# Optimization experiments

Hardware: AMD Instinct MI355X
Metric: run time of the kernel (lower is better)

## Reference

```python
import jax, jax.numpy as jnp
import numpy as np

N_NODES = 50000
N_EDGES = 800000
D_IN = 128
D_OUT = 128
BN_EPS = 1e-5


def setup_inputs() -> dict:
    key = jax.random.key(0)
    ks = jax.random.split(key, 8)
    node_feats = jax.random.normal(ks[0], (N_NODES, D_IN), dtype=jnp.float32)
    src = jax.random.randint(ks[1], (N_EDGES,), 0, N_NODES, dtype=jnp.int32)
    dst = jax.random.randint(ks[2], (N_EDGES,), 0, N_NODES, dtype=jnp.int32)
    # Glorot-ish init for weights
    scale = 1.0 / np.sqrt(D_IN)
    W = jax.random.normal(ks[3], (D_IN, D_OUT), dtype=jnp.float32) * scale
    b = jnp.zeros((D_OUT,), dtype=jnp.float32)
    Wr = jax.random.normal(ks[4], (D_IN, D_OUT), dtype=jnp.float32) * scale
    br = jnp.zeros((D_OUT,), dtype=jnp.float32)
    gamma = jnp.ones((D_OUT,), dtype=jnp.float32)
    beta = jnp.zeros((D_OUT,), dtype=jnp.float32)
    return {"node_feats": node_feats, "src": src, "dst": dst, "W": W, "b": b,
            "Wr": Wr, "br": br, "gamma": gamma, "beta": beta}


def reference(node_feats, src, dst, W, b, Wr, br, gamma, beta):
    N = node_feats.shape[0]
    ones_e = jnp.ones(src.shape[0], dtype=node_feats.dtype)
    # DGL GraphConv norm='both': D_out^{-1/2} on source side, D_in^{-1/2} on dest side
    deg_out = jnp.clip(jax.ops.segment_sum(ones_e, src, num_segments=N), 1.0)
    deg_in = jnp.clip(jax.ops.segment_sum(ones_e, dst, num_segments=N), 1.0)
    h = node_feats * jax.lax.rsqrt(deg_out)[:, None]        # [N, D_in]
    agg = jax.ops.segment_sum(h[src], dst, num_segments=N)  # gather + scatter-add, [N, D_in]
    agg = agg * jax.lax.rsqrt(deg_in)[:, None]
    gcn = jax.nn.relu(agg @ W + b)                           # GraphConv activation=relu
    res = jax.nn.relu(node_feats @ Wr + br)                  # residual branch
    y = gcn + res
    # BatchNorm1d (training mode: biased batch stats)
    mean = jnp.mean(y, axis=0)
    var = jnp.mean(jnp.square(y - mean), axis=0)
    out = (y - mean) * jax.lax.rsqrt(var + BN_EPS) * gamma + beta
    return out
```

## Files before the change

kernel.cpp:

```cpp
#include <hip/hip_runtime.h>

#define N_NODES 50000
#define N_EDGES 800000
#define D 128
#define BN_EPS 1e-5f
#define AGG_BLOCKS 2048
#define CHUNKS 64
#define EPC (N_EDGES / CHUNKS)
#define EPC4 (EPC / 4)
#define HALF_BINS 25600
#define HALF_U32 12800
#define QUART_BINS 12800
#define QUART_U32 6400
#define NB_MERGE 100

typedef short bf16x8 __attribute__((ext_vector_type(8)));
typedef float f32x4  __attribute__((ext_vector_type(4)));
typedef float f32x2  __attribute__((ext_vector_type(2)));
typedef unsigned int u32x4 __attribute__((ext_vector_type(4)));
typedef int i32x4 __attribute__((ext_vector_type(4)));


__device__ __forceinline__ unsigned int pack_rne(float a, float b) {
    unsigned int ua = __float_as_uint(a); ua += 0x7fffu + ((ua >> 16) & 1u);
    unsigned int ub = __float_as_uint(b); ub += 0x7fffu + ((ub >> 16) & 1u);
    return (ua >> 16) | (ub & 0xffff0000u);
}
__device__ __forceinline__ unsigned short pack1_rne(float a) {
    unsigned int ua = __float_as_uint(a); ua += 0x7fffu + ((ua >> 16) & 1u);
    return (unsigned short)(ua >> 16);
}
__device__ __forceinline__ unsigned char pack1_fp8(float a) {
    unsigned int u = __builtin_amdgcn_cvt_pk_fp8_f32(a, a, 0, false);
    return (unsigned char)(u & 0xffu);
}

__device__ __forceinline__ void scan_blksum(const int* __restrict__ blk_sum,
                                            int* sh, int t) {
    int v = (t < NB_MERGE) ? blk_sum[t] : 0;
    if (t < 256) sh[t] = v;
    __syncthreads();
    int inc = v;
    #pragma unroll
    for (int off = 1; off < 256; off <<= 1) {
        int u = (t >= off && t < 256) ? sh[t - off] : 0;
        __syncthreads();
        inc += u;
        if (t < 256) sh[t] = inc;
        __syncthreads();
    }
}
#define BLK_OFF(sh, mb) ((mb) ? (sh)[(mb) - 1] : 0)

__global__ __launch_bounds__(256) void hist_kernel(
        const int* __restrict__ dst, const int* __restrict__ src,
        unsigned int* __restrict__ histD, unsigned int* __restrict__ histS,
        const float* __restrict__ W, const float* __restrict__ Wr,
        uint4* __restrict__ pW, uint4* __restrict__ pWr) {
    __shared__ unsigned int h[HALF_U32];
    int tid = threadIdx.x;
    int c = blockIdx.x, r = blockIdx.y;
    if (c >= CHUNKS) {
        if (r != 0 || blockIdx.z != 0) return;
        int t = (c - CHUNKS) * 256 + tid;
        const float* S = (t & 2048) ? Wr : W;
        uint4* Dst     = (t & 2048) ? pWr : pW;
        int e = t & 2047;
        int lane = e & 63, ks = (e >> 6) & 3, ct = e >> 8;
        int n  = ct * 16 + (lane & 15);
        int k0 = ks * 32 + (lane >> 4) * 8;
        float v[8];
        #pragma unroll
        for (int j = 0; j < 8; j++) v[j] = S[(k0 + j) * D + n];
        uint4 rr;
        rr.x = pack_rne(v[0], v[1]); rr.y = pack_rne(v[2], v[3]);
        rr.z = pack_rne(v[4], v[5]); rr.w = pack_rne(v[6], v[7]);
        Dst[e] = rr;
        return;
    }
    const int* keys = blockIdx.z ? src : dst;
    unsigned int* hist = blockIdx.z ? histS : histD;
    for (int j = tid; j < HALF_U32; j += 256) h[j] = 0u;
    __syncthreads();
    int lo = r * HALF_BINS;
    const i32x4* keys4 = (const i32x4*)(keys + c * EPC);
    for (int i = tid; i < EPC4; i += 256) {
        i32x4 k = __builtin_nontemporal_load(keys4 + i);
        int b0 = k.x - lo, b1 = k.y - lo, b2 = k.z - lo, b3 = k.w - lo;
        if ((unsigned)b0 < (unsigned)HALF_BINS) atomicAdd(&h[b0 >> 1], 1u << ((b0 & 1) * 16));
        if ((unsigned)b1 < (unsigned)HALF_BINS) atomicAdd(&h[b1 >> 1], 1u << ((b1 & 1) * 16));
        if ((unsigned)b2 < (unsigned)HALF_BINS) atomicAdd(&h[b2 >> 1], 1u << ((b2 & 1) * 16));
        if ((unsigned)b3 < (unsigned)HALF_BINS) atomicAdd(&h[b3 >> 1], 1u << ((b3 & 1) * 16));
    }
    __syncthreads();
    unsigned int* out = hist + ((size_t)(r * CHUNKS + c)) * HALF_U32;
    for (int j = tid; j < HALF_U32; j += 256) out[j] = h[j];
}

__global__ __launch_bounds__(256) void merge_kernel(
        unsigned int* __restrict__ histD, unsigned int* __restrict__ histS,
        int* __restrict__ cnt_in, int* __restrict__ cnt_out,
        int* __restrict__ row_ptr, int* __restrict__ blk_sum) {
    __shared__ int sh[256];
    int t = threadIdx.x;
    int bx = blockIdx.x;
    int r = bx / 50;
    int q = (bx % 50) * 256 + t;
    int n0 = r * HALF_BINS + q * 2;
    if (blockIdx.y) {
        size_t base = (size_t)r * CHUNKS * HALF_U32 + q;
        unsigned int vals[CHUNKS];
        #pragma unroll
        for (int c = 0; c < CHUNKS; c++)
            vals[c] = histS[base + (size_t)c * HALF_U32];
        unsigned int lo = 0, hi = 0;
        #pragma unroll
        for (int c = 0; c < CHUNKS; c++) {
            lo += vals[c] & 0xffffu; hi += vals[c] >> 16;
        }
        cnt_out[n0]     = (int)lo;
        cnt_out[n0 + 1] = (int)hi;
        return;
    }
    size_t base = (size_t)r * CHUNKS * HALF_U32 + q;
    unsigned int vals[CHUNKS];
    #pragma unroll
    for (int c = 0; c < CHUNKS; c++)
        vals[c] = histD[base + (size_t)c * HALF_U32];
    unsigned int lo = 0, hi = 0;
    #pragma unroll
    for (int c = 0; c < CHUNKS; c++) {
        unsigned int v = vals[c];
        histD[base + (size_t)c * HALF_U32] = lo | (hi << 16);
        lo += v & 0xffffu; hi += v >> 16;
    }
    cnt_in[n0]     = (int)lo;
    cnt_in[n0 + 1] = (int)hi;
    int pair = (int)lo + (int)hi;
    sh[t] = pair;
    __syncthreads();
    int inc = pair;
    #pragma unroll
    for (int off = 1; off < 256; off <<= 1) {
        int u = (t >= off) ? sh[t - off] : 0;
        __syncthreads();
        inc += u; sh[t] = inc;
        __syncthreads();
    }
    int excl = inc - pair;
    row_ptr[n0]     = excl;
    row_ptr[n0 + 1] = excl + (int)lo;
    if (t == 255) blk_sum[bx] = inc;
}

__global__ __launch_bounds__(512) void fill2_kernel(
        const int* __restrict__ src, const int* __restrict__ dst,
        const int* __restrict__ row_ptr, const unsigned int* __restrict__ histP,
        const int* __restrict__ blk_sum, int* __restrict__ csr_src) {
    __shared__ unsigned int h[QUART_U32];
    __shared__ int sho[256];
    int tid = threadIdx.x;
    scan_blksum(blk_sum, sho, tid);
    int c = blockIdx.x, s = blockIdx.y;
    int base = c * EPC;
    for (int j = tid; j < QUART_U32; j += 512) h[j] = 0u;
    __syncthreads();
    int lo = s * QUART_BINS;
    int r = s >> 1;
    const unsigned int* pre_c = histP + ((size_t)(r * CHUNKS + c)) * HALF_U32
                                      + (s & 1) * QUART_U32;
    for (int i = tid; i < EPC; i += 512) {
        int d = __builtin_nontemporal_load(dst + base + i);
        int b = d - lo;
        if ((unsigned)b < (unsigned)QUART_BINS) {
            int shft = (b & 1) * 16;
            unsigned int old = atomicAdd(&h[b >> 1], 1u << shft);
            unsigned int rank = (old >> shft) & 0xffffu;
            unsigned int pre = (pre_c[b >> 1] >> shft) & 0xffffu;
            int p = row_ptr[d] + BLK_OFF(sho, d >> 9) + (int)(pre + rank);
            csr_src[p] = __builtin_nontemporal_load(src + base + i);
        }
    }
}

__global__ __launch_bounds__(256) void gemm_mfma(
        const float* __restrict__ x, const uint4* __restrict__ pW,
        const uint4* __restrict__ pWr, const float* __restrict__ br,
        const unsigned int* __restrict__ cnt_out, unsigned char* __restrict__ hwb8,
        unsigned short* __restrict__ resb) {
    __shared__ unsigned short xs[64][136];
    int tid = threadIdx.x, wid = tid >> 6, lane = tid & 63;
    int quad = lane >> 4, l15 = lane & 15;
    int r0b = blockIdx.x * 64;
    const float4* xg = (const float4*)(x + (size_t)r0b * D);
    int maxidx = (N_NODES - r0b) * (D / 4);
    #pragma unroll
    for (int i = 0; i < 8; i++) {
        int idx = tid + 256 * i;
        float4 v = (idx < maxidx) ? xg[idx] : make_float4(0.f, 0.f, 0.f, 0.f);
        int row = idx >> 5, c0 = (idx & 31) * 4;
        *(unsigned int*)&xs[row][c0]     = pack_rne(v.x, v.y);
        *(unsigned int*)&xs[row][c0 + 2] = pack_rne(v.z, v.w);
    }
    __syncthreads();
    int wrow0 = wid * 16;
    bf16x8 A[4];
    #pragma unroll
    for (int ks = 0; ks < 4; ks++)
        A[ks] = *(const bf16x8*)&xs[wrow0 + l15][ks * 32 + quad * 8];
    f32x4 accW[8], accR[8];
    #pragma unroll
    for (int ct = 0; ct < 8; ct++) { accW[ct] = (f32x4)0.f; accR[ct] = (f32x4)0.f; }
    #pragma unroll
    for (int ct = 0; ct < 8; ct++) {
        #pragma unroll
        for (int ks = 0; ks < 4; ks++) {
            union { bf16x8 v; uint4 u; } Bw, Br2;
            Bw.u  = pW [(ct * 4 + ks) * 64 + lane];
            Br2.u = pWr[(ct * 4 + ks) * 64 + lane];
            accW[ct] = __builtin_amdgcn_mfma_f32_16x16x32_bf16(A[ks], Bw.v,  accW[ct], 0, 0, 0);
            accR[ct] = __builtin_amdgcn_mfma_f32_16x16x32_bf16(A[ks], Br2.v, accR[ct], 0, 0, 0);
        }
    }
    int r0 = r0b + wrow0;
    float ro[4]; int rowok[4];
    #pragma unroll
    for (int reg = 0; reg < 4; reg++) {
        int row = r0 + quad * 4 + reg;
        rowok[reg] = row < N_NODES;
        int cw = (int)cnt_out[rowok[reg] ? row : N_NODES - 1];
        ro[reg] = rsqrtf((float)(cw > 1 ? cw : 1));
    }
    #pragma unroll
    for (int ct = 0; ct < 8; ct++) {
        int c = ct * 16 + l15;
        float brv = br[c];
        #pragma unroll
        for (int reg = 0; reg < 4; reg++) {
            int row = r0 + quad * 4 + reg;
            if (rowok[reg]) {
                hwb8[(size_t)row * D + c] = pack1_fp8(accW[ct][reg] * ro[reg]);
                resb[(size_t)row * D + c] = pack1_rne(fmaxf(accR[ct][reg] + brv, 0.f));
            }
        }
    }
}

__device__ __forceinline__ float bf_lo(unsigned int v) { return __uint_as_float(v << 16); }
__device__ __forceinline__ float bf_hi(unsigned int v) { return __uint_as_float(v & 0xffff0000u); }

__device__ __forceinline__ void acc8f8(f32x2* a, const uint2 v) {
    a[0] += __builtin_amdgcn_cvt_pk_f32_fp8(v.x, false);
    a[1] += __builtin_amdgcn_cvt_pk_f32_fp8(v.x, true);
    a[2] += __builtin_amdgcn_cvt_pk_f32_fp8(v.y, false);
    a[3] += __builtin_amdgcn_cvt_pk_f32_fp8(v.y, true);
}
__device__ __forceinline__ void acc8f8m(f32x2* a, const uint2 v, float m) {
    f32x2 m2 = {m, m};
    a[0] += m2 * __builtin_amdgcn_cvt_pk_f32_fp8(v.x, false);
    a[1] += m2 * __builtin_amdgcn_cvt_pk_f32_fp8(v.x, true);
    a[2] += m2 * __builtin_amdgcn_cvt_pk_f32_fp8(v.y, false);
    a[3] += m2 * __builtin_amdgcn_cvt_pk_f32_fp8(v.y, true);
}

__device__ __forceinline__ void gather_accum(
        const unsigned char* __restrict__ hwb8, int myidx, int cnt,
        int qg, int ql, f32x2* a) {
    int i = 0;
    for (; i + 16 <= cnt; i += 16) {
        int p0 = __shfl(myidx, i + qg);
        int p1 = __shfl(myidx, i + 4 + qg);
        int p2 = __shfl(myidx, i + 8 + qg);
        int p3 = __shfl(myidx, i + 12 + qg);
        uint2 v0 = *((const uint2*)(hwb8 + (size_t)p0 * 128) + ql);
        uint2 v1 = *((const uint2*)(hwb8 + (size_t)p1 * 128) + ql);
        uint2 v2 = *((const uint2*)(hwb8 + (size_t)p2 * 128) + ql);
        uint2 v3 = *((const uint2*)(hwb8 + (size_t)p3 * 128) + ql);
        acc8f8(a, v0); acc8f8(a, v1); acc8f8(a, v2); acc8f8(a, v3);
    }
    for (; i + 4 <= cnt; i += 4) {
        int p0 = __shfl(myidx, i + qg);
        uint2 v0 = *((const uint2*)(hwb8 + (size_t)p0 * 128) + ql);
        acc8f8(a, v0);
    }
    int t = cnt - i;
    if (t > 0) {
        int j = i + qg; if (j > cnt - 1) j = cnt - 1;
        int p0 = __shfl(myidx, j);
        uint2 v0 = *((const uint2*)(hwb8 + (size_t)p0 * 128) + ql);
        float m = (qg < t) ? 1.f : 0.f;
        acc8f8m(a, v0, m);
    }
}

__global__ __launch_bounds__(256) void agg_kernel(
        const unsigned char* __restrict__ hwb8, const int* __restrict__ row_ptr,
        const int* __restrict__ blk_sum, const unsigned int* __restrict__ cnt_in,
        const int* __restrict__ csr_src,
        const float* __restrict__ bias, const unsigned short* __restrict__ resb,
        unsigned short* __restrict__ yb, float* __restrict__ parts) {
    __shared__ float red[4 * 256];
    __shared__ int sho[256];
    int tid = threadIdx.x;
    scan_blksum(blk_sum, sho, tid);
    int lane = tid & 63, wid = tid >> 6;
    int wave = blockIdx.x * 4 + wid;
    int nw = AGG_BLOCKS * 4;
    int qg = lane >> 4;
    int ql = lane & 15;
    float s1[8] = {0,0,0,0,0,0,0,0}, s2[8] = {0,0,0,0,0,0,0,0};
    float4 bv0, bv1;
    if (lane < 16) {
        bv0 = ((const float4*)bias)[2 * lane];
        bv1 = ((const float4*)bias)[2 * lane + 1];
    }
    int n = wave;
    int e0 = 0, e1 = 0, mi = 0;
    u32x4 rv4 = (u32x4)0u;
    float ri = 0.f;
    if (n < N_NODES) {
        e0 = row_ptr[n] + BLK_OFF(sho, n >> 9);
        e1 = row_ptr[n + 1] + BLK_OFF(sho, (n + 1) >> 9);
        int ci = (int)cnt_in[n];
        ri = rsqrtf((float)(ci > 1 ? ci : 1));
        if (lane < 16) rv4 = __builtin_nontemporal_load((const u32x4*)(resb + (size_t)n * D) + lane);
        int c0 = e1 - e0; if (c0 > 64) c0 = 64;
        mi = (lane < c0) ? __builtin_nontemporal_load(csr_src + e0 + lane) : 0;
    }
    while (n < N_NODES) {
        int nn = n + nw;
        int ne0 = 0, ne1 = 0, nmi = 0;
        u32x4 nrv = (u32x4)0u;
        float nri = 0.f;
        if (nn < N_NODES) {
            ne0 = row_ptr[nn] + BLK_OFF(sho, nn >> 9);
            ne1 = row_ptr[nn + 1] + BLK_OFF(sho, (nn + 1) >> 9);
            int ci = (int)cnt_in[nn];
            nri = rsqrtf((float)(ci > 1 ? ci : 1));
            if (lane < 16) nrv = __builtin_nontemporal_load((const u32x4*)(resb + (size_t)nn * D) + lane);
            int nc = ne1 - ne0; if (nc > 64) nc = 64;
            nmi = (lane < nc) ? __builtin_nontemporal_load(csr_src + ne0 + lane) : 0;
        }
        f32x2 av[4];
        av[0] = (f32x2)0.f; av[1] = (f32x2)0.f; av[2] = (f32x2)0.f; av[3] = (f32x2)0.f;
        {
            int cnt = e1 - e0; if (cnt > 64) cnt = 64;
            gather_accum(hwb8, mi, cnt, qg, ql, av);
        }
        for (int j0 = e0 + 64; j0 < e1; j0 += 64) {
            int cnt = e1 - j0; if (cnt > 64) cnt = 64;
            int mw = (lane < cnt) ? __builtin_nontemporal_load(csr_src + j0 + lane) : 0;
            gather_accum(hwb8, mw, cnt, qg, ql, av);
        }
        float a[8] = { av[0].x, av[0].y, av[1].x, av[1].y, av[2].x, av[2].y, av[3].x, av[3].y };
        #pragma unroll
        for (int k = 0; k < 8; k++) {
            a[k] += __shfl_xor(a[k], 16);
            a[k] += __shfl_xor(a[k], 32);
        }
        if (lane < 16) {
            float o[8];
            o[0] = fmaxf(a[0] * ri + bv0.x, 0.f) + bf_lo(rv4.x);
            o[1] = fmaxf(a[1] * ri + bv0.y, 0.f) + bf_hi(rv4.x);
            o[2] = fmaxf(a[2] * ri + bv0.z, 0.f) + bf_lo(rv4.y);
            o[3] = fmaxf(a[3] * ri + bv0.w, 0.f) + bf_hi(rv4.y);
            o[4] = fmaxf(a[4] * ri + bv1.x, 0.f) + bf_lo(rv4.z);
            o[5] = fmaxf(a[5] * ri + bv1.y, 0.f) + bf_hi(rv4.z);
            o[6] = fmaxf(a[6] * ri + bv1.z, 0.f) + bf_lo(rv4.w);
            o[7] = fmaxf(a[7] * ri + bv1.w, 0.f) + bf_hi(rv4.w);
            uint4 w;
            w.x = pack_rne(o[0], o[1]); w.y = pack_rne(o[2], o[3]);
            w.z = pack_rne(o[4], o[5]); w.w = pack_rne(o[6], o[7]);
            *((uint4*)(yb + (size_t)n * D) + lane) = w;
            #pragma unroll
            for (int k = 0; k < 8; k++) { s1[k] += o[k]; s2[k] += o[k] * o[k]; }
        }
        n = nn; e0 = ne0; e1 = ne1; mi = nmi; rv4 = nrv; ri = nri;
    }
    if (lane < 16) {
        int c0 = lane * 8;
        #pragma unroll
        for (int k = 0; k < 8; k++) {
            red[wid * 256 + c0 + k]       = s1[k];
            red[wid * 256 + 128 + c0 + k] = s2[k];
        }
    }
    __syncthreads();
    if (tid < 256) {
        float v = red[tid] + red[256 + tid] + red[512 + tid] + red[768 + tid];
        parts[(size_t)blockIdx.x * 256 + tid] = v;
    }
}

__global__ __launch_bounds__(256) void bn_fin2(
        const float* __restrict__ parts, const float* __restrict__ gamma,
        const float* __restrict__ beta, float* __restrict__ scsh) {
    __shared__ float rs1[256], rs2[256];
    int c = blockIdx.x, t = threadIdx.x;
    float s1 = 0.f, s2 = 0.f;
    for (int b = t; b < AGG_BLOCKS; b += 256) {
        s1 += parts[(size_t)b * 256 + c];
        s2 += parts[(size_t)b * 256 + 128 + c];
    }
    rs1[t] = s1; rs2[t] = s2;
    __syncthreads();
    for (int off = 128; off > 0; off >>= 1) {
        if (t < off) { rs1[t] += rs1[t + off]; rs2[t] += rs2[t + off]; }
        __syncthreads();
    }
    if (t == 0) {
        const float invN = 1.0f / (float)N_NODES;
        float mean = rs1[0] * invN;
        float var  = rs2[0] * invN - mean * mean;
        float sc = gamma[c] * rsqrtf(var + BN_EPS);
        scsh[c] = sc;
        scsh[128 + c] = beta[c] - mean * sc;
    }
}

__global__ void norm_kernel(const unsigned short* __restrict__ yb,
                            const float* __restrict__ scsh, float* __restrict__ out) {
    int i = blockIdx.x * blockDim.x + threadIdx.x;
    if (i < N_NODES * 16) {
        uint4 v = ((const uint4*)yb)[i];
        int c = (i & 15) * 8;
        f32x4 o0, o1;
        o0[0] = bf_lo(v.x) * scsh[c]     + scsh[128 + c];
        o0[1] = bf_hi(v.x) * scsh[c + 1] + scsh[128 + c + 1];
        o0[2] = bf_lo(v.y) * scsh[c + 2] + scsh[128 + c + 2];
        o0[3] = bf_hi(v.y) * scsh[c + 3] + scsh[128 + c + 3];
        o1[0] = bf_lo(v.z) * scsh[c + 4] + scsh[128 + c + 4];
        o1[1] = bf_hi(v.z) * scsh[c + 5] + scsh[128 + c + 5];
        o1[2] = bf_lo(v.w) * scsh[c + 6] + scsh[128 + c + 6];
        o1[3] = bf_hi(v.w) * scsh[c + 7] + scsh[128 + c + 7];
        f32x4* ov = (f32x4*)out + (size_t)i * 2;
        __builtin_nontemporal_store(o0, ov);
        __builtin_nontemporal_store(o1, ov + 1);
    }
}

extern "C" void kernel_launch(void* const* d_in, const int* in_sizes, int n_in,
                              void* d_out, int out_size, void* d_ws, size_t ws_size,
                              hipStream_t stream) {
    const float* x     = (const float*)d_in[0];
    const int*   src   = (const int*)d_in[1];
    const int*   dst   = (const int*)d_in[2];
    const float* W     = (const float*)d_in[3];
    const float* b     = (const float*)d_in[4];
    const float* Wr    = (const float*)d_in[5];
    const float* br    = (const float*)d_in[6];
    const float* gamma = (const float*)d_in[7];
    const float* beta  = (const float*)d_in[8];
    float* out = (float*)d_out;

    char* ws = (char*)d_ws;
    int*   cnt_in  = (int*)(ws + 0);
    int*   cnt_out = (int*)(ws + 262144);
    int*   row_ptr = (int*)(ws + 524288);
    float* scsh    = (float*)(ws + 1310720);
    int*   blk_sum = (int*)(ws + 1312768);
    int*   csr_src = (int*)(ws + 1576960);
    unsigned char*  hwb8 = (unsigned char*)(ws + 4800000);
    unsigned short* resb = (unsigned short*)(ws + 11200000);
    unsigned short* yb   = (unsigned short*)(ws + 24000000);
    float* parts   = (float*)(ws + 36800000);
    uint4* pW      = (uint4*)(ws + 38897152);
    uint4* pWr     = (uint4*)(ws + 38929920);
    unsigned int* histD = (unsigned int*)(ws + 38962688);
    unsigned int* histS = (unsigned int*)(ws + 45516288);

    hist_kernel<<<dim3(CHUNKS + 16, 2, 2), 256, 0, stream>>>(
        dst, src, histD, histS, W, Wr, pW, pWr);
    merge_kernel<<<dim3(NB_MERGE, 2), 256, 0, stream>>>(
        histD, histS, (int*)cnt_in, (int*)cnt_out, row_ptr, blk_sum);
    fill2_kernel<<<dim3(CHUNKS, 4), 512, 0, stream>>>(
        src, dst, row_ptr, histD, blk_sum, csr_src);
    gemm_mfma<<<(N_NODES + 63) / 64, 256, 0, stream>>>(
        x, pW, pWr, br, (const unsigned int*)cnt_out, hwb8, resb);
    agg_kernel<<<AGG_BLOCKS, 256, 0, stream>>>(
        hwb8, row_ptr, blk_sum, (const unsigned int*)cnt_in, csr_src, b, resb, yb, parts);
    bn_fin2<<<128, 256, 0, stream>>>(parts, gamma, beta, scsh);
    norm_kernel<<<(N_NODES * 16 + 255) / 256, 256, 0, stream>>>(yb, scsh, out);
}
```

Baseline: 217.7 us.

## Split fp8 gather table into column halves and aggregate each half separately

The fp8 transformed-feature table is stored as two planes of 64 columns each instead of 128-byte rows. The aggregation kernel now runs two passes, one per half, so each pass gathers from a table half the size, which fits better in L2/MALL cache. In each gather step a wave handles 8 neighbor rows at 8 lanes per row. The cost is re-reading CSR indices, row pointers and degrees twice, an extra shuffle reduction stage, and more loop iterations per node. The output stores also become nontemporal.

```diff
diff --git a/kernel.cpp b/kernel.cpp
--- a/kernel.cpp
+++ b/kernel.cpp
@@ -13,6 +13,7 @@
 #define QUART_BINS 12800
 #define QUART_U32 6400
 #define NB_MERGE 100
+#define HWB_HALF 3200000
 
 typedef short bf16x8 __attribute__((ext_vector_type(8)));
 typedef float f32x4  __attribute__((ext_vector_type(4)));
@@ -235,11 +236,12 @@
     for (int ct = 0; ct < 8; ct++) {
         int c = ct * 16 + l15;
         float brv = br[c];
+        size_t hbase = (size_t)(c >> 6) * HWB_HALF + (size_t)(c & 63);
         #pragma unroll
         for (int reg = 0; reg < 4; reg++) {
             int row = r0 + quad * 4 + reg;
             if (rowok[reg]) {
-                hwb8[(size_t)row * D + c] = pack1_fp8(accW[ct][reg] * ro[reg]);
+                hwb8[hbase + (size_t)row * 64] = pack1_fp8(accW[ct][reg] * ro[reg]);
                 resb[(size_t)row * D + c] = pack1_rne(fmaxf(accR[ct][reg] + brv, 0.f));
             }
         }
@@ -264,30 +266,30 @@
 }
 
 __device__ __forceinline__ void gather_accum(
-        const unsigned char* __restrict__ hwb8, int myidx, int cnt,
+        const unsigned char* __restrict__ hwb, int myidx, int cnt,
         int qg, int ql, f32x2* a) {
     int i = 0;
-    for (; i + 16 <= cnt; i += 16) {
+    for (; i + 32 <= cnt; i += 32) {
         int p0 = __shfl(myidx, i + qg);
-        int p1 = __shfl(myidx, i + 4 + qg);
-        int p2 = __shfl(myidx, i + 8 + qg);
-        int p3 = __shfl(myidx, i + 12 + qg);
-        uint2 v0 = *((const uint2*)(hwb8 + (size_t)p0 * 128) + ql);
-        uint2 v1 = *((const uint2*)(hwb8 + (size_t)p1 * 128) + ql);
-        uint2 v2 = *((const uint2*)(hwb8 + (size_t)p2 * 128) + ql);
-        uint2 v3 = *((const uint2*)(hwb8 + (size_t)p3 * 128) + ql);
+        int p1 = __shfl(myidx, i + 8 + qg);
+        int p2 = __shfl(myidx, i + 16 + qg);
+        int p3 = __shfl(myidx, i + 24 + qg);
+        uint2 v0 = *((const uint2*)(hwb + (size_t)p0 * 64) + ql);
+        uint2 v1 = *((const uint2*)(hwb + (size_t)p1 * 64) + ql);
+        uint2 v2 = *((const uint2*)(hwb + (size_t)p2 * 64) + ql);
+        uint2 v3 = *((const uint2*)(hwb + (size_t)p3 * 64) + ql);
         acc8f8(a, v0); acc8f8(a, v1); acc8f8(a, v2); acc8f8(a, v3);
     }
-    for (; i + 4 <= cnt; i += 4) {
+    for (; i + 8 <= cnt; i += 8) {
         int p0 = __shfl(myidx, i + qg);
-        uint2 v0 = *((const uint2*)(hwb8 + (size_t)p0 * 128) + ql);
+        uint2 v0 = *((const uint2*)(hwb + (size_t)p0 * 64) + ql);
         acc8f8(a, v0);
     }
     int t = cnt - i;
     if (t > 0) {
         int j = i + qg; if (j > cnt - 1) j = cnt - 1;
         int p0 = __shfl(myidx, j);
-        uint2 v0 = *((const uint2*)(hwb8 + (size_t)p0 * 128) + ql);
+        uint2 v0 = *((const uint2*)(hwb + (size_t)p0 * 64) + ql);
         float m = (qg < t) ? 1.f : 0.f;
         acc8f8m(a, v0, m);
     }
@@ -306,83 +308,90 @@
     int lane = tid & 63, wid = tid >> 6;
     int wave = blockIdx.x * 4 + wid;
     int nw = AGG_BLOCKS * 4;
-    int qg = lane >> 4;
-    int ql = lane & 15;
-    float s1[8] = {0,0,0,0,0,0,0,0}, s2[8] = {0,0,0,0,0,0,0,0};
-    float4 bv0, bv1;
-    if (lane < 16) {
-        bv0 = ((const float4*)bias)[2 * lane];
-        bv1 = ((const float4*)bias)[2 * lane + 1];
-    }
-    int n = wave;
-    int e0 = 0, e1 = 0, mi = 0;
-    u32x4 rv4 = (u32x4)0u;
-    float ri = 0.f;
-    if (n < N_NODES) {
-        e0 = row_ptr[n] + BLK_OFF(sho, n >> 9);
-        e1 = row_ptr[n + 1] + BLK_OFF(sho, (n + 1) >> 9);
-        int ci = (int)cnt_in[n];
-        ri = rsqrtf((float)(ci > 1 ? ci : 1));
-        if (lane < 16) rv4 = __builtin_nontemporal_load((const u32x4*)(resb + (size_t)n * D) + lane);
-        int c0 = e1 - e0; if (c0 > 64) c0 = 64;
-        mi = (lane < c0) ? __builtin_nontemporal_load(csr_src + e0 + lane) : 0;
-    }
-    while (n < N_NODES) {
-        int nn = n + nw;
-        int ne0 = 0, ne1 = 0, nmi = 0;
-        u32x4 nrv = (u32x4)0u;
-        float nri = 0.f;
-        if (nn < N_NODES) {
-            ne0 = row_ptr[nn] + BLK_OFF(sho, nn >> 9);
-            ne1 = row_ptr[nn + 1] + BLK_OFF(sho, (nn + 1) >> 9);
-            int ci = (int)cnt_in[nn];
-            nri = rsqrtf((float)(ci > 1 ? ci : 1));
-            if (lane < 16) nrv = __builtin_nontemporal_load((const u32x4*)(resb + (size_t)nn * D) + lane);
-            int nc = ne1 - ne0; if (nc > 64) nc = 64;
-            nmi = (lane < nc) ? __builtin_nontemporal_load(csr_src + ne0 + lane) : 0;
-        }
-        f32x2 av[4];
-        av[0] = (f32x2)0.f; av[1] = (f32x2)0.f; av[2] = (f32x2)0.f; av[3] = (f32x2)0.f;
-        {
-            int cnt = e1 - e0; if (cnt > 64) cnt = 64;
-            gather_accum(hwb8, mi, cnt, qg, ql, av);
-        }
-        for (int j0 = e0 + 64; j0 < e1; j0 += 64) {
-            int cnt = e1 - j0; if (cnt > 64) cnt = 64;
-            int mw = (lane < cnt) ? __builtin_nontemporal_load(csr_src + j0 + lane) : 0;
-            gather_accum(hwb8, mw, cnt, qg, ql, av);
-        }
-        float a[8] = { av[0].x, av[0].y, av[1].x, av[1].y, av[2].x, av[2].y, av[3].x, av[3].y };
-        #pragma unroll
-        for (int k = 0; k < 8; k++) {
-            a[k] += __shfl_xor(a[k], 16);
-            a[k] += __shfl_xor(a[k], 32);
-        }
-        if (lane < 16) {
-            float o[8];
-            o[0] = fmaxf(a[0] * ri + bv0.x, 0.f) + bf_lo(rv4.x);
-            o[1] = fmaxf(a[1] * ri + bv0.y, 0.f) + bf_hi(rv4.x);
-            o[2] = fmaxf(a[2] * ri + bv0.z, 0.f) + bf_lo(rv4.y);
-            o[3] = fmaxf(a[3] * ri + bv0.w, 0.f) + bf_hi(rv4.y);
-            o[4] = fmaxf(a[4] * ri + bv1.x, 0.f) + bf_lo(rv4.z);
-            o[5] = fmaxf(a[5] * ri + bv1.y, 0.f) + bf_hi(rv4.z);
-            o[6] = fmaxf(a[6] * ri + bv1.z, 0.f) + bf_lo(rv4.w);
-            o[7] = fmaxf(a[7] * ri + bv1.w, 0.f) + bf_hi(rv4.w);
-            uint4 w;
-            w.x = pack_rne(o[0], o[1]); w.y = pack_rne(o[2], o[3]);
-            w.z = pack_rne(o[4], o[5]); w.w = pack_rne(o[6], o[7]);
-            *((uint4*)(yb + (size_t)n * D) + lane) = w;
+    int qg = lane >> 3;
+    int ql = lane & 7;
+    for (int half = 0; half < 2; half++) {
+        const unsigned char* hwb = hwb8 + (size_t)half * HWB_HALF;
+        float s1[8] = {0,0,0,0,0,0,0,0}, s2[8] = {0,0,0,0,0,0,0,0};
+        float4 bv0, bv1;
+        if (lane < 8) {
+            bv0 = ((const float4*)(bias + half * 64))[2 * ql];
+            bv1 = ((const float4*)(bias + half * 64))[2 * ql + 1];
+        }
+        int n = wave;
+        int e0 = 0, e1 = 0, mi = 0;
+        u32x4 rv4 = (u32x4)0u;
+        float ri = 0.f;
+        if (n < N_NODES) {
+            e0 = row_ptr[n] + BLK_OFF(sho, n >> 9);
+            e1 = row_ptr[n + 1] + BLK_OFF(sho, (n + 1) >> 9);
+            int ci = (int)cnt_in[n];
+            ri = rsqrtf((float)(ci > 1 ? ci : 1));
+            if (lane < 8) rv4 = __builtin_nontemporal_load(
+                (const u32x4*)(resb + (size_t)n * D + half * 64) + ql);
+            int c0 = e1 - e0; if (c0 > 64) c0 = 64;
+            mi = (lane < c0) ? __builtin_nontemporal_load(csr_src + e0 + lane) : 0;
+        }
+        while (n < N_NODES) {
+            int nn = n + nw;
+            int ne0 = 0, ne1 = 0, nmi = 0;
+            u32x4 nrv = (u32x4)0u;
+            float nri = 0.f;
+            if (nn < N_NODES) {
+                ne0 = row_ptr[nn] + BLK_OFF(sho, nn >> 9);
+                ne1 = row_ptr[nn + 1] + BLK_OFF(sho, (nn + 1) >> 9);
+                int ci = (int)cnt_in[nn];
+                nri = rsqrtf((float)(ci > 1 ? ci : 1));
+                if (lane < 8) nrv = __builtin_nontemporal_load(
+                    (const u32x4*)(resb + (size_t)nn * D + half * 64) + ql);
+                int nc = ne1 - ne0; if (nc > 64) nc = 64;
+                nmi = (lane < nc) ? __builtin_nontemporal_load(csr_src + ne0 + lane) : 0;
+            }
+            f32x2 av[4];
+            av[0] = (f32x2)0.f; av[1] = (f32x2)0.f; av[2] = (f32x2)0.f; av[3] = (f32x2)0.f;
+            {
+                int cnt = e1 - e0; if (cnt > 64) cnt = 64;
+                gather_accum(hwb, mi, cnt, qg, ql, av);
+            }
+            for (int j0 = e0 + 64; j0 < e1; j0 += 64) {
+                int cnt = e1 - j0; if (cnt > 64) cnt = 64;
+                int mw = (lane < cnt) ? __builtin_nontemporal_load(csr_src + j0 + lane) : 0;
+                gather_accum(hwb, mw, cnt, qg, ql, av);
+            }
+            float a[8] = { av[0].x, av[0].y, av[1].x, av[1].y, av[2].x, av[2].y, av[3].x, av[3].y };
             #pragma unroll
-            for (int k = 0; k < 8; k++) { s1[k] += o[k]; s2[k] += o[k] * o[k]; }
-        }
-        n = nn; e0 = ne0; e1 = ne1; mi = nmi; rv4 = nrv; ri = nri;
-    }
-    if (lane < 16) {
-        int c0 = lane * 8;
-        #pragma unroll
-        for (int k = 0; k < 8; k++) {
-            red[wid * 256 + c0 + k]       = s1[k];
-            red[wid * 256 + 128 + c0 + k] = s2[k];
+            for (int k = 0; k < 8; k++) {
+                a[k] += __shfl_xor(a[k], 8);
+                a[k] += __shfl_xor(a[k], 16);
+                a[k] += __shfl_xor(a[k], 32);
+            }
+            if (lane < 8) {
+                float o[8];
+                o[0] = fmaxf(a[0] * ri + bv0.x, 0.f) + bf_lo(rv4.x);
+                o[1] = fmaxf(a[1] * ri + bv0.y, 0.f) + bf_hi(rv4.x);
+                o[2] = fmaxf(a[2] * ri + bv0.z, 0.f) + bf_lo(rv4.y);
+                o[3] = fmaxf(a[3] * ri + bv0.w, 0.f) + bf_hi(rv4.y);
+                o[4] = fmaxf(a[4] * ri + bv1.x, 0.f) + bf_lo(rv4.z);
+                o[5] = fmaxf(a[5] * ri + bv1.y, 0.f) + bf_hi(rv4.z);
+                o[6] = fmaxf(a[6] * ri + bv1.z, 0.f) + bf_lo(rv4.w);
+                o[7] = fmaxf(a[7] * ri + bv1.w, 0.f) + bf_hi(rv4.w);
+                u32x4 w;
+                w.x = pack_rne(o[0], o[1]); w.y = pack_rne(o[2], o[3]);
+                w.z = pack_rne(o[4], o[5]); w.w = pack_rne(o[6], o[7]);
+                __builtin_nontemporal_store(w,
+                    (u32x4*)(yb + (size_t)n * D + half * 64) + ql);
+                #pragma unroll
+                for (int k = 0; k < 8; k++) { s1[k] += o[k]; s2[k] += o[k] * o[k]; }
+            }
+            n = nn; e0 = ne0; e1 = ne1; mi = nmi; rv4 = nrv; ri = nri;
+        }
+        if (lane < 8) {
+            int c0 = half * 64 + ql * 8;
+            #pragma unroll
+            for (int k = 0; k < 8; k++) {
+                red[wid * 256 + c0 + k]       = s1[k];
+                red[wid * 256 + 128 + c0 + k] = s2[k];
+            }
         }
     }
     __syncthreads();
```

Result: slower. 248.1 us (+13.9%).

## Deepen aggregation pipeline: prefetch next node's first 16 gathered rows

Applied to the files above, without the earlier changes.

Makes the per-wave node loop software-pipelined two nodes deep. Index and metadata loads run two iterations ahead, and the first 16 fp8 neighbor-row gathers of the next node are issued before the current node's gather is accumulated. This is meant to hide the latency of the dependent csr_src→hwb8 gather chain, at the cost of extra registers, which may lower occupancy. Masked clamped loads handle nodes with fewer than 16 edges.

```diff
diff --git a/kernel.cpp b/kernel.cpp
--- a/kernel.cpp
+++ b/kernel.cpp
@@ -261,6 +261,61 @@
     a[1] += m2 * __builtin_amdgcn_cvt_pk_f32_fp8(v.x, true);
     a[2] += m2 * __builtin_amdgcn_cvt_pk_f32_fp8(v.y, false);
     a[3] += m2 * __builtin_amdgcn_cvt_pk_f32_fp8(v.y, true);
+}
+
+__device__ __forceinline__ void prefetch16(
+        const unsigned char* __restrict__ hwb8, int myidx, int cnt,
+        int qg, int ql,
+        uint2& v0, uint2& v1, uint2& v2, uint2& v3,
+        float& m0, float& m1, float& m2, float& m3) {
+    int cm = cnt - 1; if (cm < 0) cm = 0;
+    int j0 = qg,      j1 = 4 + qg, j2 = 8 + qg, j3 = 12 + qg;
+    m0 = (j0 < cnt) ? 1.f : 0.f;
+    m1 = (j1 < cnt) ? 1.f : 0.f;
+    m2 = (j2 < cnt) ? 1.f : 0.f;
+    m3 = (j3 < cnt) ? 1.f : 0.f;
+    if (j0 > cm) j0 = cm;
+    if (j1 > cm) j1 = cm;
+    if (j2 > cm) j2 = cm;
+    if (j3 > cm) j3 = cm;
+    int p0 = __shfl(myidx, j0);
+    int p1 = __shfl(myidx, j1);
+    int p2 = __shfl(myidx, j2);
+    int p3 = __shfl(myidx, j3);
+    v0 = *((const uint2*)(hwb8 + (size_t)p0 * 128) + ql);
+    v1 = *((const uint2*)(hwb8 + (size_t)p1 * 128) + ql);
+    v2 = *((const uint2*)(hwb8 + (size_t)p2 * 128) + ql);
+    v3 = *((const uint2*)(hwb8 + (size_t)p3 * 128) + ql);
+}
+
+__device__ __forceinline__ void gather_rest(
+        const unsigned char* __restrict__ hwb8, int myidx, int cnt,
+        int qg, int ql, f32x2* a) {
+    int i = 16;
+    for (; i + 16 <= cnt; i += 16) {
+        int p0 = __shfl(myidx, i + qg);
+        int p1 = __shfl(myidx, i + 4 + qg);
+        int p2 = __shfl(myidx, i + 8 + qg);
+        int p3 = __shfl(myidx, i + 12 + qg);
+        uint2 v0 = *((const uint2*)(hwb8 + (size_t)p0 * 128) + ql);
+        uint2 v1 = *((const uint2*)(hwb8 + (size_t)p1 * 128) + ql);
+        uint2 v2 = *((const uint2*)(hwb8 + (size_t)p2 * 128) + ql);
+        uint2 v3 = *((const uint2*)(hwb8 + (size_t)p3 * 128) + ql);
+        acc8f8(a, v0); acc8f8(a, v1); acc8f8(a, v2); acc8f8(a, v3);
+    }
+    for (; i + 4 <= cnt; i += 4) {
+        int p0 = __shfl(myidx, i + qg);
+        uint2 v0 = *((const uint2*)(hwb8 + (size_t)p0 * 128) + ql);
+        acc8f8(a, v0);
+    }
+    int t = cnt - i;
+    if (t > 0) {
+        int j = i + qg; if (j > cnt - 1) j = cnt - 1;
+        int p0 = __shfl(myidx, j);
+        uint2 v0 = *((const uint2*)(hwb8 + (size_t)p0 * 128) + ql);
+        float m = (qg < t) ? 1.f : 0.f;
+        acc8f8m(a, v0, m);
+    }
 }
 
 __device__ __forceinline__ void gather_accum(
@@ -314,41 +369,60 @@
         bv0 = ((const float4*)bias)[2 * lane];
         bv1 = ((const float4*)bias)[2 * lane + 1];
     }
+    int e0_0 = 0, e1_0 = 0, mi_0 = 0; float ri_0 = 0.f; u32x4 rv_0 = (u32x4)0u;
+    int e0_1 = 0, e1_1 = 0, mi_1 = 0; float ri_1 = 0.f; u32x4 rv_1 = (u32x4)0u;
+    uint2 pv0, pv1, pv2, pv3; float pm0 = 0.f, pm1 = 0.f, pm2 = 0.f, pm3 = 0.f;
+    pv0 = pv1 = pv2 = pv3 = make_uint2(0u, 0u);
+
     int n = wave;
-    int e0 = 0, e1 = 0, mi = 0;
-    u32x4 rv4 = (u32x4)0u;
-    float ri = 0.f;
     if (n < N_NODES) {
-        e0 = row_ptr[n] + BLK_OFF(sho, n >> 9);
-        e1 = row_ptr[n + 1] + BLK_OFF(sho, (n + 1) >> 9);
+        e0_0 = row_ptr[n] + BLK_OFF(sho, n >> 9);
+        e1_0 = row_ptr[n + 1] + BLK_OFF(sho, (n + 1) >> 9);
         int ci = (int)cnt_in[n];
-        ri = rsqrtf((float)(ci > 1 ? ci : 1));
-        if (lane < 16) rv4 = __builtin_nontemporal_load((const u32x4*)(resb + (size_t)n * D) + lane);
-        int c0 = e1 - e0; if (c0 > 64) c0 = 64;
-        mi = (lane < c0) ? __builtin_nontemporal_load(csr_src + e0 + lane) : 0;
-    }
+        ri_0 = rsqrtf((float)(ci > 1 ? ci : 1));
+        if (lane < 16) rv_0 = __builtin_nontemporal_load((const u32x4*)(resb + (size_t)n * D) + lane);
+        int c0 = e1_0 - e0_0; if (c0 > 64) c0 = 64;
+        mi_0 = (lane < c0) ? __builtin_nontemporal_load(csr_src + e0_0 + lane) : 0;
+        prefetch16(hwb8, mi_0, c0, qg, ql, pv0, pv1, pv2, pv3, pm0, pm1, pm2, pm3);
+    }
+    int n1g = n + nw;
+    if (n1g < N_NODES) {
+        e0_1 = row_ptr[n1g] + BLK_OFF(sho, n1g >> 9);
+        e1_1 = row_ptr[n1g + 1] + BLK_OFF(sho, (n1g + 1) >> 9);
+        int ci = (int)cnt_in[n1g];
+        ri_1 = rsqrtf((float)(ci > 1 ? ci : 1));
+        if (lane < 16) rv_1 = __builtin_nontemporal_load((const u32x4*)(resb + (size_t)n1g * D) + lane);
+        int c1 = e1_1 - e0_1; if (c1 > 64) c1 = 64;
+        mi_1 = (lane < c1) ? __builtin_nontemporal_load(csr_src + e0_1 + lane) : 0;
+    }
+
     while (n < N_NODES) {
-        int nn = n + nw;
-        int ne0 = 0, ne1 = 0, nmi = 0;
-        u32x4 nrv = (u32x4)0u;
-        float nri = 0.f;
-        if (nn < N_NODES) {
-            ne0 = row_ptr[nn] + BLK_OFF(sho, nn >> 9);
-            ne1 = row_ptr[nn + 1] + BLK_OFF(sho, (nn + 1) >> 9);
-            int ci = (int)cnt_in[nn];
-            nri = rsqrtf((float)(ci > 1 ? ci : 1));
-            if (lane < 16) nrv = __builtin_nontemporal_load((const u32x4*)(resb + (size_t)nn * D) + lane);
-            int nc = ne1 - ne0; if (nc > 64) nc = 64;
-            nmi = (lane < nc) ? __builtin_nontemporal_load(csr_src + ne0 + lane) : 0;
+        int n2 = n + 2 * nw;
+        int e0_2 = 0, e1_2 = 0, mi_2 = 0; float ri_2 = 0.f; u32x4 rv_2 = (u32x4)0u;
+        if (n2 < N_NODES) {
+            e0_2 = row_ptr[n2] + BLK_OFF(sho, n2 >> 9);
+            e1_2 = row_ptr[n2 + 1] + BLK_OFF(sho, (n2 + 1) >> 9);
+            int ci = (int)cnt_in[n2];
+            ri_2 = rsqrtf((float)(ci > 1 ? ci : 1));
+            if (lane < 16) rv_2 = __builtin_nontemporal_load((const u32x4*)(resb + (size_t)n2 * D) + lane);
+            int c2 = e1_2 - e0_2; if (c2 > 64) c2 = 64;
+            mi_2 = (lane < c2) ? __builtin_nontemporal_load(csr_src + e0_2 + lane) : 0;
+        }
+        uint2 qv0, qv1, qv2, qv3; float qm0, qm1, qm2, qm3;
+        {
+            int c1 = e1_1 - e0_1; if (c1 > 64) c1 = 64;
+            prefetch16(hwb8, mi_1, c1, qg, ql, qv0, qv1, qv2, qv3, qm0, qm1, qm2, qm3);
         }
         f32x2 av[4];
         av[0] = (f32x2)0.f; av[1] = (f32x2)0.f; av[2] = (f32x2)0.f; av[3] = (f32x2)0.f;
+        acc8f8m(av, pv0, pm0); acc8f8m(av, pv1, pm1);
+        acc8f8m(av, pv2, pm2); acc8f8m(av, pv3, pm3);
         {
-            int cnt = e1 - e0; if (cnt > 64) cnt = 64;
-            gather_accum(hwb8, mi, cnt, qg, ql, av);
-        }
-        for (int j0 = e0 + 64; j0 < e1; j0 += 64) {
-            int cnt = e1 - j0; if (cnt > 64) cnt = 64;
+            int cnt = e1_0 - e0_0; if (cnt > 64) cnt = 64;
+            gather_rest(hwb8, mi_0, cnt, qg, ql, av);
+        }
+        for (int j0 = e0_0 + 64; j0 < e1_0; j0 += 64) {
+            int cnt = e1_0 - j0; if (cnt > 64) cnt = 64;
             int mw = (lane < cnt) ? __builtin_nontemporal_load(csr_src + j0 + lane) : 0;
             gather_accum(hwb8, mw, cnt, qg, ql, av);
         }
@@ -360,14 +434,14 @@
         }
         if (lane < 16) {
             float o[8];
-            o[0] = fmaxf(a[0] * ri + bv0.x, 0.f) + bf_lo(rv4.x);
-            o[1] = fmaxf(a[1] * ri + bv0.y, 0.f) + bf_hi(rv4.x);
-            o[2] = fmaxf(a[2] * ri + bv0.z, 0.f) + bf_lo(rv4.y);
-            o[3] = fmaxf(a[3] * ri + bv0.w, 0.f) + bf_hi(rv4.y);
-            o[4] = fmaxf(a[4] * ri + bv1.x, 0.f) + bf_lo(rv4.z);
-            o[5] = fmaxf(a[5] * ri + bv1.y, 0.f) + bf_hi(rv4.z);
-            o[6] = fmaxf(a[6] * ri + bv1.z, 0.f) + bf_lo(rv4.w);
-            o[7] = fmaxf(a[7] * ri + bv1.w, 0.f) + bf_hi(rv4.w);
+            o[0] = fmaxf(a[0] * ri_0 + bv0.x, 0.f) + bf_lo(rv_0.x);
+            o[1] = fmaxf(a[1] * ri_0 + bv0.y, 0.f) + bf_hi(rv_0.x);
+            o[2] = fmaxf(a[2] * ri_0 + bv0.z, 0.f) + bf_lo(rv_0.y);
+            o[3] = fmaxf(a[3] * ri_0 + bv0.w, 0.f) + bf_hi(rv_0.y);
+            o[4] = fmaxf(a[4] * ri_0 + bv1.x, 0.f) + bf_lo(rv_0.z);
+            o[5] = fmaxf(a[5] * ri_0 + bv1.y, 0.f) + bf_hi(rv_0.z);
+            o[6] = fmaxf(a[6] * ri_0 + bv1.z, 0.f) + bf_lo(rv_0.w);
+            o[7] = fmaxf(a[7] * ri_0 + bv1.w, 0.f) + bf_hi(rv_0.w);
             uint4 w;
             w.x = pack_rne(o[0], o[1]); w.y = pack_rne(o[2], o[3]);
             w.z = pack_rne(o[4], o[5]); w.w = pack_rne(o[6], o[7]);
@@ -375,7 +449,11 @@
             #pragma unroll
             for (int k = 0; k < 8; k++) { s1[k] += o[k]; s2[k] += o[k] * o[k]; }
         }
-        n = nn; e0 = ne0; e1 = ne1; mi = nmi; rv4 = nrv; ri = nri;
+        n += nw;
+        e0_0 = e0_1; e1_0 = e1_1; mi_0 = mi_1; ri_0 = ri_1; rv_0 = rv_1;
+        e0_1 = e0_2; e1_1 = e1_2; mi_1 = mi_2; ri_1 = ri_2; rv_1 = rv_2;
+        pv0 = qv0; pv1 = qv1; pv2 = qv2; pv3 = qv3;
+        pm0 = qm0; pm1 = qm1; pm2 = qm2; pm3 = qm3;
     }
     if (lane < 16) {
         int c0 = lane * 8;
```

Result: faster. 211.9 us (-2.7%).
